# Kernel optimization log

Hardware: AMD Instinct MI355X
Metric: run time of the kernel (lower is better)

## Reference

```python
import jax, jax.numpy as jnp
import numpy as np

# init_kwargs (defaults)
COST_CLASS = 1.0
COST_BBOX = 1.0
COST_GIOU = 1.0

B, Q, T, C = 64, 900, 100, 256
INF = 1e9


def box_cxcywh_to_xyxy(b):
    cx, cy, w, h = jnp.split(b, 4, axis=-1)
    return jnp.concatenate([cx - 0.5 * w, cy - 0.5 * h, cx + 0.5 * w, cy + 0.5 * h], axis=-1)


def pairwise_giou(a, b):
    # a: [Q,4], b: [T,4] in xyxy -> [Q,T] generalized IoU
    area_a = (a[:, 2] - a[:, 0]) * (a[:, 3] - a[:, 1])
    area_b = (b[:, 2] - b[:, 0]) * (b[:, 3] - b[:, 1])
    lt = jnp.maximum(a[:, None, :2], b[None, :, :2])
    rb = jnp.minimum(a[:, None, 2:], b[None, :, 2:])
    wh = jnp.clip(rb - lt, 0.0)
    inter = wh[..., 0] * wh[..., 1]
    union = area_a[:, None] + area_b[None, :] - inter
    iou = inter / union
    lt_e = jnp.minimum(a[:, None, :2], b[None, :, :2])
    rb_e = jnp.maximum(a[:, None, 2:], b[None, :, 2:])
    wh_e = jnp.clip(rb_e - lt_e, 0.0)
    enclose = wh_e[..., 0] * wh_e[..., 1]
    return iou - (enclose - union) / enclose


def cost_matrix(pred_logits, pred_boxes, tgt_labels, tgt_boxes):
    # NOTE: the original module indexes RAW logits (out_prob softmax is computed but unused)
    cost_class = -jax.vmap(lambda L, t: L[:, t])(pred_logits, tgt_labels)        # [B,Q,T]
    cost_bbox = jnp.abs(pred_boxes[:, :, None, :] - tgt_boxes[:, None, :, :]).sum(-1)  # L1 cdist [B,Q,T]
    cost_giou = -jax.vmap(pairwise_giou)(box_cxcywh_to_xyxy(pred_boxes), box_cxcywh_to_xyxy(tgt_boxes))
    return COST_CLASS * cost_class + COST_BBOX * cost_bbox + COST_GIOU * cost_giou


def hungarian(cost):
    """Exact Hungarian (shortest augmenting path / Jonker-Volgenant) on cost [T, Q], T<=Q.
    Returns col[T]: the column (query) optimally assigned to each row (target)."""
    Tn, Qn = cost.shape
    i32 = jnp.int32

    def assign_row(carry, i):
        u, v, p = carry                       # duals u:[T+1], v:[Q+1]; p[j]=row matched to col j (-1 free)
        p = p.at[Qn].set(i)                   # virtual start column Qn holds current row
        init = (u, v, p,
                jnp.full((Qn,), INF, cost.dtype),     # minv: shortest slack to each column
                jnp.zeros((Qn + 1,), bool),           # used columns (alternating tree)
                jnp.zeros((Qn,), i32),                # way: predecessor column
                i32(Qn))                              # j0: current column

        def cond(s):
            _, _, p_, _, _, _, j0 = s
            return p_[j0] >= 0

        def body(s):
            u_, v_, p_, minv, used, way, j0 = s
            used = used.at[j0].set(True)
            i0 = p_[j0]
            cur = cost[i0] - u_[i0] - v_[:Qn]
            free = ~used[:Qn]
            better = (cur < minv) & free
            minv = jnp.where(better, cur, minv)
            way = jnp.where(better, j0, way)
            masked = jnp.where(free, minv, INF)
            j1 = jnp.argmin(masked).astype(i32)
            delta = masked[j1]
            rows = jnp.where(used, p_, Tn)    # dump unused into scratch slot Tn
            u_ = u_.at[rows].add(delta)
            v_ = jnp.where(used, v_ - delta, v_)
            minv = jnp.where(free, minv - delta, minv)
            return (u_, v_, p_, minv, used, way, j1)

        u, v, p, _, _, way, j0 = jax.lax.while_loop(cond, body, init)

        def aug_body(s):
            p_, j0_ = s
            j1 = way[j0_]
            return (p_.at[j0_].set(p_[j1]), j1)

        p, _ = jax.lax.while_loop(lambda s: s[1] != Qn, aug_body, (p, j0))
        return (u, v, p), None

    u0 = jnp.zeros((Tn + 1,), cost.dtype)
    v0 = jnp.zeros((Qn + 1,), cost.dtype)
    p0 = jnp.full((Qn + 1,), -1, i32)
    (_, _, p), _ = jax.lax.scan(assign_row, (u0, v0, p0), jnp.arange(Tn, dtype=i32))
    rows = jnp.where(p[:Qn] >= 0, p[:Qn], Tn)
    col = jnp.zeros((Tn + 1,), i32).at[rows].set(jnp.arange(Qn, dtype=i32))
    return col[:Tn]


def setup_inputs() -> dict:
    key = jax.random.key(0)
    k1, k2, k3, k4 = jax.random.split(key, 4)
    return {
        "pred_logits": jax.random.normal(k1, (B, Q, C), jnp.float32),
        "pred_boxes": jax.random.uniform(k2, (B, Q, 4), jnp.float32, 0.05, 0.95),  # cxcywh in (0,1)
        "tgt_labels": jax.random.randint(k3, (B, T), 0, C, jnp.int32),
        "tgt_boxes": jax.random.uniform(k4, (B, T, 4), jnp.float32, 0.05, 0.95),
    }


def reference(pred_logits, pred_boxes, tgt_labels, tgt_boxes):
    cost = cost_matrix(pred_logits, pred_boxes, tgt_labels, tgt_boxes)   # [B,Q,T]
    col = jax.vmap(hungarian)(jnp.swapaxes(cost, 1, 2))                   # [B,T] query per target
    # present like scipy: pred indices sorted ascending, with matching target indices
    order = jnp.argsort(col, axis=1)                                      # [B,T]
    pred_idx = jnp.take_along_axis(col, order, axis=1)
    tgt_idx = order.astype(jnp.int32)
    return cost, pred_idx, tgt_idx
```

## Files before the change

kernel.cpp:

```cpp
#include <hip/hip_runtime.h>
#include <stdint.h>

#define B_ 64
#define Q_ 900
#define T_ 100
#define C_ 256
#define INF_ 1e9f
#define QT 32
#define NQB 29
#define NG 8
#define TPG 13
#define SC 101
#define KSLOT 15
#define RG 4
#define NW 8
#define HB 512

#define DPP_STEP_F(x, ctrl, rmask)                                             \
    x = fminf(x, __int_as_float(__builtin_amdgcn_update_dpp(                   \
            0x7F800000 , __float_as_int(x), ctrl, rmask, 0xF, false)))
#define DPP_STEP_I(x, ctrl, rmask)                                             \
    x = min(x, __builtin_amdgcn_update_dpp(                                    \
            0x7FFFFFFF, x, ctrl, rmask, 0xF, false))

__device__ __forceinline__ float wave_min_bcast_f(float x) {
    DPP_STEP_F(x, 0x111, 0xF);
    DPP_STEP_F(x, 0x112, 0xF);
    DPP_STEP_F(x, 0x114, 0xF);
    DPP_STEP_F(x, 0x118, 0xF);
    DPP_STEP_F(x, 0x142, 0xA);
    DPP_STEP_F(x, 0x143, 0xC);
    return __int_as_float(__builtin_amdgcn_readlane(__float_as_int(x), 63));
}
__device__ __forceinline__ int wave_min_bcast_i(int x) {
    DPP_STEP_I(x, 0x111, 0xF);
    DPP_STEP_I(x, 0x112, 0xF);
    DPP_STEP_I(x, 0x114, 0xF);
    DPP_STEP_I(x, 0x118, 0xF);
    DPP_STEP_I(x, 0x142, 0xA);
    DPP_STEP_I(x, 0x143, 0xC);
    return __builtin_amdgcn_readlane(x, 63);
}

__global__ __launch_bounds__(256) void cost_kernel(
    const float* __restrict__ logits,
    const float* __restrict__ pboxes,
    const int*   __restrict__ tlabels,
    const float* __restrict__ tboxes,
    float* __restrict__ cost_out,
    float* __restrict__ costT_out)
{
    const int b   = blockIdx.y;
    const int q0  = blockIdx.x * QT;
    const int tid = threadIdx.x;

    __shared__ float  s_log[QT][C_ + 1];
    __shared__ float  s_c[QT][SC];
    __shared__ float4 s_tb4[T_];
    __shared__ int    s_lab[T_];

    if (tid < T_) {
        s_tb4[tid] = *reinterpret_cast<const float4*>(tboxes + ((size_t)b * T_ + tid) * 4);
        s_lab[tid] = tlabels[b * T_ + tid];
    }

    const float* __restrict__ lgb = logits + (size_t)b * Q_ * C_;
    #pragma unroll
    for (int it = 0; it < 8; ++it) {
        const int idx = it * 256 + tid;
        const int row = (idx >> 4) & 31;
        const int c4  = (idx & 15) | ((idx >> 9) << 4);
        const int q   = q0 + row;
        float4 vv = make_float4(0.f, 0.f, 0.f, 0.f);
        if (q < Q_)
            vv = *reinterpret_cast<const float4*>(lgb + (size_t)q * C_ + (c4 << 2));
        float* d = &s_log[row][c4 << 2];
        d[0] = vv.x; d[1] = vv.y; d[2] = vv.z; d[3] = vv.w;
    }
    __syncthreads();

    const int qr  = tid & 31;
    const int q   = q0 + qr;
    const bool qok = (q < Q_);
    const int qc  = qok ? q : (Q_ - 1);
    const int g   = tid >> 5;

    const float4 pb = *reinterpret_cast<const float4*>(pboxes + ((size_t)b * Q_ + qc) * 4);
    const float pcx = pb.x, pcy = pb.y, pw = pb.z, ph = pb.w;
    const float ax0 = pcx - 0.5f * pw, ay0 = pcy - 0.5f * ph;
    const float ax1 = pcx + 0.5f * pw, ay1 = pcy + 0.5f * ph;
    const float area_a = (ax1 - ax0) * (ay1 - ay0);

    const float* __restrict__ srow = s_log[qr];
    const int tbase = g * TPG;
    const int tcnt  = (T_ - tbase < TPG) ? (T_ - tbase) : TPG;

    float c[TPG];
    #pragma unroll
    for (int k = 0; k < TPG; ++k) {
        const int t = tbase + ((k < tcnt) ? k : 0);
        const float4 tb = s_tb4[t];
        const float cls = -srow[s_lab[t]];
        const float l1 = fabsf(pcx - tb.x) + fabsf(pcy - tb.y)
                       + fabsf(pw  - tb.z) + fabsf(ph  - tb.w);
        const float bx0 = tb.x - 0.5f * tb.z, by0 = tb.y - 0.5f * tb.w;
        const float bx1 = tb.x + 0.5f * tb.z, by1 = tb.y + 0.5f * tb.w;
        const float area_b = (bx1 - bx0) * (by1 - by0);
        const float ltx = fmaxf(ax0, bx0), lty = fmaxf(ay0, by0);
        const float rbx = fminf(ax1, bx1), rby = fminf(ay1, by1);
        const float wx = fmaxf(rbx - ltx, 0.0f), wy = fmaxf(rby - lty, 0.0f);
        const float inter = wx * wy;
        const float uni = area_a + area_b - inter;
        const float iou = inter / uni;
        const float ex0 = fminf(ax0, bx0), ey0 = fminf(ay0, by0);
        const float ex1 = fmaxf(ax1, bx1), ey1 = fmaxf(ay1, by1);
        const float ew = fmaxf(ex1 - ex0, 0.0f), eh = fmaxf(ey1 - ey0, 0.0f);
        const float enc = ew * eh;
        const float giou = iou - (enc - uni) / enc;
        c[k] = cls + l1 - giou;
    }

    if (qok) {
        float* __restrict__ ct = costT_out + (size_t)b * T_ * Q_ + (size_t)tbase * Q_ + q;
        #pragma unroll
        for (int k = 0; k < TPG; ++k)
            if (k < tcnt) ct[(size_t)k * Q_] = c[k];

        #pragma unroll
        for (int k = 0; k < TPG; ++k)
            if (k < tcnt) s_c[qr][tbase + k] = c[k];
    }
    __syncthreads();

    const int nrows = (Q_ - q0 < QT) ? (Q_ - q0) : QT;
    const int ntot  = nrows * T_;
    float* __restrict__ tile = cost_out + ((size_t)b * Q_ + q0) * T_;
    for (int idx = tid; idx < ntot; idx += 256) {
        const int r = idx / T_;
        const int t = idx - r * T_;
        tile[idx] = s_c[r][t];
    }
}

__global__ __launch_bounds__(HB) void hung_kernel(
    const float* __restrict__ costT,
    float* __restrict__ out_pred,
    float* __restrict__ out_tgt)
{
    const int b    = blockIdx.x;
    const int tid  = threadIdx.x;
    const int lane = tid & 63;
    const int wave = tid >> 6;
    const float* __restrict__ cb = costT + (size_t)b * T_ * Q_;

    __shared__ float u[128];
    __shared__ float v[Q_];
    __shared__ int   p[Q_];
    __shared__ int   way_priv[NW][Q_];
    __shared__ int   ji[T_];
    __shared__ int   s_pend[T_];
    __shared__ int   col[T_];
    __shared__ int   s_mask[NW][64];
    __shared__ int   s_qn, s_acc;

    for (int j = tid; j < Q_; j += HB) {
        p[j] = -1; v[j] = 0.0f; way_priv[0][j] = 0x7FFFFFFF;
    }
    if (tid >= 100 && tid < 128) u[tid] = INF_;

    for (int g = wave * RG; g < T_; g += NW * RG) {
        float rv[RG][KSLOT];
        #pragma unroll
        for (int r = 0; r < RG; ++r) {
            const float* __restrict__ row = cb + (size_t)(g + r) * Q_;
            #pragma unroll
            for (int k = 0; k < KSLOT; ++k) {
                int j = k * 64 + lane;
                rv[r][k] = (j < Q_) ? row[j] : INF_;
            }
        }
        #pragma unroll
        for (int r = 0; r < RG; ++r) {
            float m = INF_; int mj = Q_;
            #pragma unroll
            for (int k = 0; k < KSLOT; ++k) {
                int j = k * 64 + lane;
                if (rv[r][k] < m) { m = rv[r][k]; mj = j; }
            }
            const float mm = wave_min_bcast_f(m);
            const int   gj = wave_min_bcast_i((m == mm) ? mj : 0x7FFFFFFF);
            if (lane == 0) { u[g + r] = mm; ji[g + r] = gj; }
        }
    }
    __syncthreads();

    if (wave == 0) {
        int t0 = lane, t1 = lane + 64;
        if (t0 < T_) atomicMin(&way_priv[0][ji[t0]], t0);
        if (t1 < T_) atomicMin(&way_priv[0][ji[t1]], t1);
        bool lose0 = false, lose1 = false;
        if (t0 < T_) {
            int j = ji[t0];
            if (way_priv[0][j] == t0) p[j] = t0; else lose0 = true;
        }
        if (t1 < T_) {
            int j = ji[t1];
            if (way_priv[0][j] == t1) p[j] = t1; else lose1 = true;
        }
        unsigned long long m0 = __ballot(lose0);
        unsigned long long m1 = __ballot(lose1);
        const int c0 = __popcll(m0);
        if (lose0) s_pend[__popcll(m0 & ((1ull << lane) - 1ull))] = lane;
        if (lose1) s_pend[c0 + __popcll(m1 & ((1ull << lane) - 1ull))] = lane + 64;
        if (lane == 0) s_qn = c0 + __popcll(m1);
    }

    for (;;) {
        __syncthreads();
        const int qn = s_qn;
        if (qn <= 0) break;
        const int nact   = (qn < NW) ? qn : NW;
        const bool active = (wave < nact);
        const int  isrc   = active ? s_pend[wave] : -1;

        const float u_lo = u[lane];
        const float u_hi = u[64 + lane];
        float vreg[KSLOT];
        #pragma unroll
        for (int k = 0; k < KSLOT; ++k) {
            int j = k * 64 + lane;
            vreg[k] = (j < Q_) ? v[j] : 0.0f;
        }

        unsigned int used = 0;
        float vadd[KSLOT], minv[KSLOT];
        float uisrc_acc = 0.0f;
        int jfin = Q_;

        if (active) {
            int* __restrict__ wayw = way_priv[wave];
            #pragma unroll
            for (int k = 0; k < KSLOT; ++k) { minv[k] = INF_; vadd[k] = 0.0f; }
            int j0 = Q_;
            uisrc_acc = u[isrc];
            float uicur = uisrc_acc;

            float pre[KSLOT];
            {
                const float* __restrict__ row = cb + (size_t)isrc * Q_;
                #pragma unroll
                for (int k = 0; k < KSLOT; ++k) {
                    int j = k * 64 + lane;
                    pre[k] = (j < Q_) ? row[j] : INF_;
                }
            }

            while (true) {
                float best = INF_; int bj = Q_;
                #pragma unroll
                for (int k = 0; k < KSLOT; ++k) {
                    int j = k * 64 + lane;
                    if (j < Q_ && !((used >> k) & 1u)) {
                        float cur = pre[k] - uicur - vreg[k];
                        if (cur < minv[k]) { minv[k] = cur; wayw[j] = j0; }
                        float mm = minv[k];
                        if (mm < best) { best = mm; bj = j; }
                    }
                }
                const float delta = wave_min_bcast_f(best);
                const int   j1    = wave_min_bcast_i((best == delta) ? bj : 0x7FFFFFFF);
                const int   inext = p[j1];

                {
                    int ipre = (inext < 0) ? 0 : inext;
                    const float* __restrict__ row = cb + (size_t)ipre * Q_;
                    #pragma unroll
                    for (int k = 0; k < KSLOT; ++k) {
                        int j = k * 64 + lane;
                        pre[k] = (j < Q_) ? row[j] : INF_;
                    }
                }

                uisrc_acc += delta;
                #pragma unroll
                for (int k = 0; k < KSLOT; ++k) {
                    int j = k * 64 + lane;
                    if (j < Q_) {
                        if ((used >> k) & 1u) vadd[k] += delta;
                        else                  minv[k] -= delta;
                    }
                }

                if (inext < 0) { jfin = j1; break; }

                if (lane == (j1 & 63)) used |= 1u << (j1 >> 6);
                {
                    const int si = __builtin_amdgcn_readfirstlane(inext);
                    const float tsel = (si < 64) ? u_lo : u_hi;
                    uicur = __int_as_float(
                        __builtin_amdgcn_readlane(__float_as_int(tsel), si & 63));
                }
                j0 = j1;
            }
        }

        {
            int msk = active ? (int)used : 0;
            if (active && lane == (jfin & 63)) msk |= 1 << (jfin >> 6);
            s_mask[wave][lane] = msk;
        }
        __syncthreads();

        if (wave == 0) {
            int acc = 1;
            for (int bb = 1; bb < nact; ++bb) {
                int mb = s_mask[bb][lane];
                bool ok = true;
                for (int aa = 0; aa < bb; ++aa) {
                    if ((acc >> aa) & 1) {
                        bool hit = (s_mask[aa][lane] & mb) != 0;
                        if (__ballot(hit) != 0ull) ok = false;
                    }
                }
                if (ok) acc |= 1 << bb;
            }
            if (lane == 0) s_acc = acc;
        }
        __syncthreads();

        if (active && ((s_acc >> wave) & 1)) {
            #pragma unroll
            for (int k = 0; k < KSLOT; ++k) {
                int j = k * 64 + lane;
                if (j < Q_ && ((used >> k) & 1u)) {
                    int r = p[j];
                    u[r] = u[r] + vadd[k];
                    v[j] = v[j] - vadd[k];
                }
            }
            if (lane == 0) {
                u[isrc] = uisrc_acc;
                int jj = jfin;
                int* __restrict__ wayw = way_priv[wave];
                while (true) {
                    int jp = wayw[jj];
                    if (jp == Q_) { p[jj] = isrc; break; }
                    p[jj] = p[jp];
                    jj = jp;
                }
            }
        }
        __syncthreads();

        if (tid == 0) {
            int acc = s_acc;
            int tmp[NW]; int nrej = 0;
            for (int w = 0; w < nact; ++w)
                if (!((acc >> w) & 1)) tmp[nrej++] = s_pend[w];
            for (int i = 0; i < nrej; ++i) s_pend[i] = tmp[i];
            for (int i = nact; i < qn; ++i) s_pend[nrej + i - nact] = s_pend[i];
            s_qn = qn - nact + nrej;
        }
    }

    for (int j = tid; j < Q_; j += HB) {
        int r = p[j];
        if (r >= 0) col[r] = j;
    }
    __syncthreads();
    if (tid < T_) {
        int cj = col[tid];
        int rank = 0;
        for (int t2 = 0; t2 < T_; ++t2) rank += (col[t2] < cj) ? 1 : 0;
        out_pred[b * T_ + rank] = (float)cj;
        out_tgt [b * T_ + rank] = (float)tid;
    }
}

extern "C" void kernel_launch(void* const* d_in, const int* in_sizes, int n_in,
                              void* d_out, int out_size, void* d_ws, size_t ws_size,
                              hipStream_t stream) {
    const float* logits  = (const float*)d_in[0];
    const float* pboxes  = (const float*)d_in[1];
    const int*   tlabels = (const int*)d_in[2];
    const float* tboxes  = (const float*)d_in[3];

    float* out      = (float*)d_out;
    float* cost     = out;
    float* out_pred = out + (size_t)B_ * Q_ * T_;
    float* out_tgt  = out_pred + (size_t)B_ * T_;

    float* costT = (float*)d_ws;

    dim3 gridc(NQB, B_);
    cost_kernel<<<gridc, 256, 0, stream>>>(logits, pboxes, tlabels, tboxes, cost, costT);
    hung_kernel<<<B_, HB, 0, stream>>>(costT, out_pred, out_tgt);
}
```

Baseline: 149.8 us.

## Make cost kernel persistent over query tiles with register-prefetched logits

The cost kernel now launches 12 blocks per batch instead of 29, and each block walks 2–3 query tiles. The logits and pred boxes for the next tile are prefetched into registers while the current tile is computed, then written to shared memory after a barrier. The aim is to hide global load latency and spread the per-block setup of target boxes and labels over several tiles. In exchange there are fewer blocks, so less occupancy and parallelism, plus an extra barrier per tile and higher register pressure. The Hungarian kernel, which probably dominates total time, is unchanged.

```diff
diff --git a/kernel.cpp b/kernel.cpp
--- a/kernel.cpp
+++ b/kernel.cpp
@@ -7,7 +7,7 @@
 #define C_ 256
 #define INF_ 1e9f
 #define QT 32
-#define NQB 29
+#define TBLK 12
 #define NG 8
 #define TPG 13
 #define SC 101
@@ -51,7 +51,7 @@
     float* __restrict__ costT_out)
 {
     const int b   = blockIdx.y;
-    const int q0  = blockIdx.x * QT;
+    const int bx  = blockIdx.x;
     const int tid = threadIdx.x;
 
     __shared__ float  s_log[QT][C_ + 1];
@@ -65,80 +65,128 @@
     }
 
     const float* __restrict__ lgb = logits + (size_t)b * Q_ * C_;
+    const int nt = (bx < 5) ? 3 : 2;
+    const int qr = tid & 31;
+    const int g  = tid >> 5;
+    const int tbase = g * TPG;
+    const int tcnt  = (T_ - tbase < TPG) ? (T_ - tbase) : TPG;
+
+    int srow_[8], sc4_[8];
     #pragma unroll
     for (int it = 0; it < 8; ++it) {
         const int idx = it * 256 + tid;
-        const int row = (idx >> 4) & 31;
-        const int c4  = (idx & 15) | ((idx >> 9) << 4);
-        const int q   = q0 + row;
-        float4 vv = make_float4(0.f, 0.f, 0.f, 0.f);
-        if (q < Q_)
-            vv = *reinterpret_cast<const float4*>(lgb + (size_t)q * C_ + (c4 << 2));
-        float* d = &s_log[row][c4 << 2];
-        d[0] = vv.x; d[1] = vv.y; d[2] = vv.z; d[3] = vv.w;
+        srow_[it] = (idx >> 4) & 31;
+        sc4_[it]  = (idx & 15) | ((idx >> 9) << 4);
+    }
+
+    float4 rr[8];
+    float4 pbc, pbn;
+
+    {
+        const int q0 = bx * QT;
+        #pragma unroll
+        for (int it = 0; it < 8; ++it) {
+            const int q = q0 + srow_[it];
+            rr[it] = (q < Q_)
+                ? *reinterpret_cast<const float4*>(lgb + (size_t)q * C_ + (sc4_[it] << 2))
+                : make_float4(0.f, 0.f, 0.f, 0.f);
+        }
+        const int q  = q0 + qr;
+        const int qc = (q < Q_) ? q : (Q_ - 1);
+        pbc = *reinterpret_cast<const float4*>(pboxes + ((size_t)b * Q_ + qc) * 4);
+        #pragma unroll
+        for (int it = 0; it < 8; ++it) {
+            float* d = &s_log[srow_[it]][sc4_[it] << 2];
+            d[0] = rr[it].x; d[1] = rr[it].y; d[2] = rr[it].z; d[3] = rr[it].w;
+        }
     }
     __syncthreads();
 
-    const int qr  = tid & 31;
-    const int q   = q0 + qr;
-    const bool qok = (q < Q_);
-    const int qc  = qok ? q : (Q_ - 1);
-    const int g   = tid >> 5;
-
-    const float4 pb = *reinterpret_cast<const float4*>(pboxes + ((size_t)b * Q_ + qc) * 4);
-    const float pcx = pb.x, pcy = pb.y, pw = pb.z, ph = pb.w;
-    const float ax0 = pcx - 0.5f * pw, ay0 = pcy - 0.5f * ph;
-    const float ax1 = pcx + 0.5f * pw, ay1 = pcy + 0.5f * ph;
-    const float area_a = (ax1 - ax0) * (ay1 - ay0);
-
-    const float* __restrict__ srow = s_log[qr];
-    const int tbase = g * TPG;
-    const int tcnt  = (T_ - tbase < TPG) ? (T_ - tbase) : TPG;
-
-    float c[TPG];
-    #pragma unroll
-    for (int k = 0; k < TPG; ++k) {
-        const int t = tbase + ((k < tcnt) ? k : 0);
-        const float4 tb = s_tb4[t];
-        const float cls = -srow[s_lab[t]];
-        const float l1 = fabsf(pcx - tb.x) + fabsf(pcy - tb.y)
-                       + fabsf(pw  - tb.z) + fabsf(ph  - tb.w);
-        const float bx0 = tb.x - 0.5f * tb.z, by0 = tb.y - 0.5f * tb.w;
-        const float bx1 = tb.x + 0.5f * tb.z, by1 = tb.y + 0.5f * tb.w;
-        const float area_b = (bx1 - bx0) * (by1 - by0);
-        const float ltx = fmaxf(ax0, bx0), lty = fmaxf(ay0, by0);
-        const float rbx = fminf(ax1, bx1), rby = fminf(ay1, by1);
-        const float wx = fmaxf(rbx - ltx, 0.0f), wy = fmaxf(rby - lty, 0.0f);
-        const float inter = wx * wy;
-        const float uni = area_a + area_b - inter;
-        const float iou = inter / uni;
-        const float ex0 = fminf(ax0, bx0), ey0 = fminf(ay0, by0);
-        const float ex1 = fmaxf(ax1, bx1), ey1 = fmaxf(ay1, by1);
-        const float ew = fmaxf(ex1 - ex0, 0.0f), eh = fmaxf(ey1 - ey0, 0.0f);
-        const float enc = ew * eh;
-        const float giou = iou - (enc - uni) / enc;
-        c[k] = cls + l1 - giou;
-    }
-
-    if (qok) {
-        float* __restrict__ ct = costT_out + (size_t)b * T_ * Q_ + (size_t)tbase * Q_ + q;
-        #pragma unroll
-        for (int k = 0; k < TPG; ++k)
-            if (k < tcnt) ct[(size_t)k * Q_] = c[k];
-
-        #pragma unroll
-        for (int k = 0; k < TPG; ++k)
-            if (k < tcnt) s_c[qr][tbase + k] = c[k];
-    }
-    __syncthreads();
-
-    const int nrows = (Q_ - q0 < QT) ? (Q_ - q0) : QT;
-    const int ntot  = nrows * T_;
-    float* __restrict__ tile = cost_out + ((size_t)b * Q_ + q0) * T_;
-    for (int idx = tid; idx < ntot; idx += 256) {
-        const int r = idx / T_;
-        const int t = idx - r * T_;
-        tile[idx] = s_c[r][t];
+    for (int i = 0; i < nt; ++i) {
+        const int q0  = (bx + TBLK * i) * QT;
+        const int q   = q0 + qr;
+        const bool qok = (q < Q_);
+        const bool more = (i + 1 < nt);
+
+        if (more) {
+            const int q0n = (bx + TBLK * (i + 1)) * QT;
+            #pragma unroll
+            for (int it = 0; it < 8; ++it) {
+                const int qn = q0n + srow_[it];
+                rr[it] = (qn < Q_)
+                    ? *reinterpret_cast<const float4*>(lgb + (size_t)qn * C_ + (sc4_[it] << 2))
+                    : make_float4(0.f, 0.f, 0.f, 0.f);
+            }
+            const int qn  = q0n + qr;
+            const int qcn = (qn < Q_) ? qn : (Q_ - 1);
+            pbn = *reinterpret_cast<const float4*>(pboxes + ((size_t)b * Q_ + qcn) * 4);
+        }
+
+        const float pcx = pbc.x, pcy = pbc.y, pw = pbc.z, ph = pbc.w;
+        const float ax0 = pcx - 0.5f * pw, ay0 = pcy - 0.5f * ph;
+        const float ax1 = pcx + 0.5f * pw, ay1 = pcy + 0.5f * ph;
+        const float area_a = (ax1 - ax0) * (ay1 - ay0);
+        const float* __restrict__ srow = s_log[qr];
+
+        float c[TPG];
+        #pragma unroll
+        for (int k = 0; k < TPG; ++k) {
+            const int t = tbase + ((k < tcnt) ? k : 0);
+            const float4 tb = s_tb4[t];
+            const float cls = -srow[s_lab[t]];
+            const float l1 = fabsf(pcx - tb.x) + fabsf(pcy - tb.y)
+                           + fabsf(pw  - tb.z) + fabsf(ph  - tb.w);
+            const float bx0 = tb.x - 0.5f * tb.z, by0 = tb.y - 0.5f * tb.w;
+            const float bx1 = tb.x + 0.5f * tb.z, by1 = tb.y + 0.5f * tb.w;
+            const float area_b = (bx1 - bx0) * (by1 - by0);
+            const float ltx = fmaxf(ax0, bx0), lty = fmaxf(ay0, by0);
+            const float rbx = fminf(ax1, bx1), rby = fminf(ay1, by1);
+            const float wx = fmaxf(rbx - ltx, 0.0f), wy = fmaxf(rby - lty, 0.0f);
+            const float inter = wx * wy;
+            const float uni = area_a + area_b - inter;
+            const float iou = inter / uni;
+            const float ex0 = fminf(ax0, bx0), ey0 = fminf(ay0, by0);
+            const float ex1 = fmaxf(ax1, bx1), ey1 = fmaxf(ay1, by1);
+            const float ew = fmaxf(ex1 - ex0, 0.0f), eh = fmaxf(ey1 - ey0, 0.0f);
+            const float enc = ew * eh;
+            const float giou = iou - (enc - uni) / enc;
+            c[k] = cls + l1 - giou;
+        }
+
+        if (qok) {
+            float* __restrict__ ct = costT_out + (size_t)b * T_ * Q_ + (size_t)tbase * Q_ + q;
+            #pragma unroll
+            for (int k = 0; k < TPG; ++k)
+                if (k < tcnt) ct[(size_t)k * Q_] = c[k];
+        }
+
+        __syncthreads();
+
+        if (qok) {
+            #pragma unroll
+            for (int k = 0; k < TPG; ++k)
+                if (k < tcnt) s_c[qr][tbase + k] = c[k];
+        }
+        if (more) {
+            #pragma unroll
+            for (int it = 0; it < 8; ++it) {
+                float* d = &s_log[srow_[it]][sc4_[it] << 2];
+                d[0] = rr[it].x; d[1] = rr[it].y; d[2] = rr[it].z; d[3] = rr[it].w;
+            }
+        }
+
+        __syncthreads();
+
+        const int nrows = (Q_ - q0 < QT) ? (Q_ - q0) : QT;
+        const int ntot  = nrows * T_;
+        float* __restrict__ tile = cost_out + ((size_t)b * Q_ + q0) * T_;
+        for (int idx = tid; idx < ntot; idx += 256) {
+            const int r = idx / T_;
+            const int t = idx - r * T_;
+            tile[idx] = s_c[r][t];
+        }
+
+        pbc = pbn;
     }
 }
 
@@ -392,7 +440,7 @@
 
     float* costT = (float*)d_ws;
 
-    dim3 gridc(NQB, B_);
+    dim3 gridc(TBLK, B_);
     cost_kernel<<<gridc, 256, 0, stream>>>(logits, pboxes, tlabels, tboxes, cost, costT);
     hung_kernel<<<B_, HB, 0, stream>>>(costT, out_pred, out_tgt);
 }
```

Measured after the change: 141.3 us. 1.06x faster.
